# Kernel optimization log

Hardware: AMD Instinct MI355X
Metric: run time of the kernel (lower is better)

Reference implementation:

```python
import jax, jax.numpy as jnp
import numpy as np

N_NODES = 100000
N_EDGES = 1600000
IN_FEATS = 256
NUM_HEADS = 4
OUT_FEATS = 64
NEG_SLOPE = 0.2


def setup_inputs() -> dict:
    key = jax.random.key(0)
    k1, k2, k3, k4, k5, k6 = jax.random.split(key, 6)
    feat = jax.random.normal(k1, (N_NODES, IN_FEATS), dtype=jnp.float32)
    # VarianceScaling(scale=sqrt(2), fan_avg) ~ std = sqrt(2*sqrt(2)/(fan_in+fan_out))
    w_std = float(np.sqrt(np.sqrt(2.0) * 2.0 / (IN_FEATS + NUM_HEADS * OUT_FEATS)))
    W = jax.random.normal(k2, (IN_FEATS, NUM_HEADS * OUT_FEATS), dtype=jnp.float32) * w_std
    a_std = float(np.sqrt(np.sqrt(2.0) * 2.0 / (1 + OUT_FEATS)))
    attn_l = jax.random.normal(k3, (1, NUM_HEADS, OUT_FEATS), dtype=jnp.float32) * a_std
    attn_r = jax.random.normal(k4, (1, NUM_HEADS, OUT_FEATS), dtype=jnp.float32) * a_std
    src = jax.random.randint(k5, (N_EDGES,), 0, N_NODES, dtype=jnp.int32)
    dst = jax.random.randint(k6, (N_EDGES,), 0, N_NODES, dtype=jnp.int32)
    return {"feat": feat, "W": W, "attn_l": attn_l, "attn_r": attn_r, "src": src, "dst": dst}


def reference(feat, W, attn_l, attn_r, src, dst):
    N = feat.shape[0]
    H, D = attn_l.shape[1], attn_l.shape[2]
    # projection: [N, H, D]
    ft = jnp.reshape(feat @ W, (N, H, D))
    # per-node attention logits: [N, H]
    el = jnp.sum(ft * attn_l, axis=-1)
    er = jnp.sum(ft * attn_r, axis=-1)
    # per-edge logits (u_add_v) + LeakyReLU: [E, H]
    e = jax.nn.leaky_relu(el[src] + er[dst], negative_slope=NEG_SLOPE)
    # segmented softmax over incoming edges of each destination node
    seg_max = jax.ops.segment_max(e, dst, num_segments=N)  # [N, H]
    seg_max = jnp.where(jnp.isfinite(seg_max), seg_max, 0.0)
    ex = jnp.exp(e - seg_max[dst])  # [E, H]
    seg_sum = jax.ops.segment_sum(ex, dst, num_segments=N)  # [N, H]
    a = ex / seg_sum[dst]  # [E, H]
    # weighted scatter-sum aggregation (u_mul_e then sum): [N, H, D]
    msgs = ft[src] * a[:, :, None]  # [E, H, D]
    rst = jax.ops.segment_sum(msgs, dst, num_segments=N)
    return rst
```

## Files before the change

### kernel.cpp

```cpp
#include <hip/hip_runtime.h>

#define HEADS 4
#define DH 64
#define NHID 256
#define KIN 256
#define NEG_SLOPE 0.2f
#define CAP 128
#define EPB 2048

typedef __attribute__((ext_vector_type(8))) short short8;
typedef __attribute__((ext_vector_type(4))) float f32x4;

__device__ inline float bf2f(unsigned short u) {
  union { unsigned int i; float f; } v; v.i = ((unsigned int)u) << 16; return v.f;
}
__device__ inline unsigned short f2bf(float f) {
  union { float f; unsigned int i; } v; v.f = f;
  unsigned int r = v.i + 0x7FFF + ((v.i >> 16) & 1);
  return (unsigned short)(r >> 16);
}

__global__ void k_cvtW(const float* __restrict__ W, unsigned short* __restrict__ Wt,
                       int* __restrict__ deg, int M) {
  int n = blockIdx.x, k = threadIdx.x;
  Wt[n * 256 + k] = f2bf(W[k * 256 + n]);
  for (int i = blockIdx.x * 256 + threadIdx.x; i < M; i += 256 * 256) deg[i] = 0;
}

__global__ __launch_bounds__(256, 2) void k_fillgemm(
    const float* __restrict__ feat, const unsigned short* __restrict__ Wt,
    const float* __restrict__ al, const float* __restrict__ ar,
    unsigned short* __restrict__ ftb, float* __restrict__ el,
    float* __restrict__ er, int M,
    const int* __restrict__ src, const int* __restrict__ dst,
    int* __restrict__ deg, int* __restrict__ bucket, int E)
{
  __shared__ unsigned short As[64 * 256];
  __shared__ unsigned short Bs[2][256 * 32];
  const int t = threadIdx.x;
  const int b = blockIdx.x;
  const int q = b / 3, rmd = b % 3;

  if (rmd == 0) {
    int e0 = q * EPB + t;
    #pragma unroll
    for (int j = 0; j < 8; ++j) {
      int e = e0 + j * 256;
      if (e < E) {
        int d = __builtin_nontemporal_load(dst + e);
        int s = __builtin_nontemporal_load(src + e);
        int p = atomicAdd(&deg[d], 1);
        bucket[(size_t)d * CAP + p] = s;
      }
    }
    return;
  }

  const int gi = b - q - 1;
  const int lane = t & 63;
  const int w = t >> 6;
  const int row0 = gi * 64;

  f32x4 acc[4][4] = {};

  f32x4 av0[8], av1[8];
  #pragma unroll
  for (int j = 0; j < 8; ++j) {
    int g = j * 256 + t;
    int r = g >> 5, c = g & 31;
    const f32x4* ga = (const f32x4*)(feat + (size_t)min(row0 + r, M - 1) * KIN + c * 8);
    av0[j] = __builtin_nontemporal_load(ga);
    av1[j] = __builtin_nontemporal_load(ga + 1);
  }
  const int bn0 = t >> 2, bkc = t & 3;
  #pragma unroll
  for (int j = 0; j < 4; ++j) {
    int n = j * 64 + bn0;
    const unsigned short* gb = Wt + n * 256 + ((bkc ^ ((n >> 1) & 3)) * 8);
    __builtin_amdgcn_global_load_lds(
        (const __attribute__((address_space(1))) void*)gb,
        (__attribute__((address_space(3))) void*)((char*)Bs[0] + j * 4096 + t * 16),
        16, 0, 0);
  }
  #pragma unroll
  for (int j = 0; j < 8; ++j) {
    int g = j * 256 + t;
    int r = g >> 5, c = g & 31;
    short8 pk;
    pk[0] = (short)f2bf(av0[j][0]); pk[1] = (short)f2bf(av0[j][1]);
    pk[2] = (short)f2bf(av0[j][2]); pk[3] = (short)f2bf(av0[j][3]);
    pk[4] = (short)f2bf(av1[j][0]); pk[5] = (short)f2bf(av1[j][1]);
    pk[6] = (short)f2bf(av1[j][2]); pk[7] = (short)f2bf(av1[j][3]);
    *(short8*)((char*)As + r * 512 + ((c ^ (r & 7)) * 16)) = pk;
  }
  __syncthreads();

  const int i = lane & 15, kc = lane >> 4;
  for (int kt = 0; kt < 8; ++kt) {
    if (kt < 7) {
      int k0 = (kt + 1) * 32;
      #pragma unroll
      for (int j = 0; j < 4; ++j) {
        int n = j * 64 + bn0;
        const unsigned short* gb = Wt + n * 256 + k0 + ((bkc ^ ((n >> 1) & 3)) * 8);
        __builtin_amdgcn_global_load_lds(
            (const __attribute__((address_space(1))) void*)gb,
            (__attribute__((address_space(3))) void*)((char*)Bs[(kt + 1) & 1] + j * 4096 + t * 16),
            16, 0, 0);
      }
    }
    short8 af[4], bf[4];
    #pragma unroll
    for (int m = 0; m < 4; ++m) {
      int r = m * 16 + i;
      int c = kt * 4 + kc;
      af[m] = *(const short8*)((const char*)As + r * 512 + ((c ^ (r & 7)) * 16));
    }
    const char* bbase = (const char*)Bs[kt & 1];
    #pragma unroll
    for (int n = 0; n < 4; ++n) {
      int nr = w * 64 + n * 16 + i;
      bf[n] = *(const short8*)(bbase + nr * 64 + ((kc ^ ((nr >> 1) & 3)) * 16));
    }
    #pragma unroll
    for (int m = 0; m < 4; ++m)
      #pragma unroll
      for (int n = 0; n < 4; ++n)
        acc[m][n] = __builtin_amdgcn_mfma_f32_16x16x32_bf16(af[m], bf[n], acc[m][n], 0, 0, 0);
    __syncthreads();
  }

  const int ci = lane & 15, rg = lane >> 4;
  #pragma unroll
  for (int m = 0; m < 4; ++m) {
    #pragma unroll
    for (int r = 0; r < 4; ++r) {
      int grow = row0 + m * 16 + rg * 4 + r;
      if (grow < M) {
        unsigned short* fp = ftb + (size_t)grow * NHID + w * 64;
        #pragma unroll
        for (int n = 0; n < 4; ++n) fp[n * 16 + ci] = f2bf(acc[m][n][r]);
      }
    }
  }
  float alv[4], arv[4];
  #pragma unroll
  for (int n = 0; n < 4; ++n) {
    alv[n] = al[w * DH + n * 16 + ci];
    arv[n] = ar[w * DH + n * 16 + ci];
  }
  #pragma unroll
  for (int m = 0; m < 4; ++m) {
    #pragma unroll
    for (int r = 0; r < 4; ++r) {
      float pl = 0.f, pr = 0.f;
      #pragma unroll
      for (int n = 0; n < 4; ++n) {
        pl += acc[m][n][r] * alv[n];
        pr += acc[m][n][r] * arv[n];
      }
      pl += __shfl_xor(pl, 1); pl += __shfl_xor(pl, 2);
      pl += __shfl_xor(pl, 4); pl += __shfl_xor(pl, 8);
      pr += __shfl_xor(pr, 1); pr += __shfl_xor(pr, 2);
      pr += __shfl_xor(pr, 4); pr += __shfl_xor(pr, 8);
      if (ci == 0) {
        int grow = row0 + m * 16 + rg * 4 + r;
        if (grow < M) { el[grow * HEADS + w] = pl; er[grow * HEADS + w] = pr; }
      }
    }
  }
}

__global__ __launch_bounds__(256) void k_aggr(
    const unsigned short* __restrict__ ftb, const float* __restrict__ el,
    const float* __restrict__ er, const int* __restrict__ deg,
    const int* __restrict__ bucket, float* __restrict__ out, int N)
{
  int n = blockIdx.x * 4 + (threadIdx.x >> 6);
  int lane = threadIdx.x & 63;
  if (n >= N) return;
  int q  = lane >> 4;
  int ql = lane & 15;
  int hh = ql >> 2;
  int start = n * CAP;
  int end = start + deg[n];
  const short8* ft8 = (const short8*)ftb;
  float acc[16] = {};
  float ws = 0.f;
  if (end > start) {
    float erh = er[n * HEADS + hh];
    int last = end - 1;
    int eA = start + q;
    int eB = eA + 4;
    int sB = bucket[min(eB, last)];
    {
      int sA = bucket[min(eA, last)];
      float lxA = el[sA * 4 + hh];
      short8 fa0 = ft8[(size_t)sA * 32 + ql * 2];
      short8 fa1 = ft8[(size_t)sA * 32 + ql * 2 + 1];
      for (int e0 = start; e0 < end; e0 += 4) {
        int sC = bucket[min(e0 + 8 + q, last)];
        float lxB = el[sB * 4 + hh];
        short8 fb0 = ft8[(size_t)sB * 32 + ql * 2];
        short8 fb1 = ft8[(size_t)sB * 32 + ql * 2 + 1];
        bool v = (e0 + q) < end;
        float x = lxA + erh;
        x = x > 0.f ? x : NEG_SLOPE * x;
        float ex = v ? __expf(x) : 0.f;
        ws += ex;
        #pragma unroll
        for (int j = 0; j < 8; ++j) acc[j]     += ex * bf2f((unsigned short)fa0[j]);
        #pragma unroll
        for (int j = 0; j < 8; ++j) acc[j + 8] += ex * bf2f((unsigned short)fa1[j]);
        sB = sC; lxA = lxB; fa0 = fb0; fa1 = fb1;
      }
    }
  }
  ws += __shfl_xor(ws, 16); ws += __shfl_xor(ws, 32);
  #pragma unroll
  for (int j = 0; j < 16; ++j) {
    acc[j] += __shfl_xor(acc[j], 16);
    acc[j] += __shfl_xor(acc[j], 32);
  }
  if (q == 0) {
    float inv = (end > start) ? 1.f / ws : 0.f;
    float* op = out + (size_t)n * NHID + ql * 16;
    #pragma unroll
    for (int j4 = 0; j4 < 4; ++j4)
      *(float4*)(op + j4 * 4) = make_float4(acc[j4 * 4] * inv, acc[j4 * 4 + 1] * inv,
                                            acc[j4 * 4 + 2] * inv, acc[j4 * 4 + 3] * inv);
  }
}

extern "C" void kernel_launch(void* const* d_in, const int* in_sizes, int n_in,
                              void* d_out, int out_size, void* d_ws, size_t ws_size,
                              hipStream_t stream)
{
  const float* feat = (const float*)d_in[0];
  const float* W    = (const float*)d_in[1];
  const float* al   = (const float*)d_in[2];
  const float* ar   = (const float*)d_in[3];
  const int*   src  = (const int*)d_in[4];
  const int*   dst  = (const int*)d_in[5];
  const int M = in_sizes[0] / KIN;
  const int E = in_sizes[4];
  float* out = (float*)d_out;

  char* base = (char*)d_ws;
  size_t off = 0;
  auto alloc = [&](size_t b) { char* p = base + off; off = (off + b + 255) & ~(size_t)255; return p; };
  unsigned short* ftb = (unsigned short*)alloc((size_t)M * NHID * sizeof(unsigned short));
  unsigned short* Wt  = (unsigned short*)alloc(256 * 256 * sizeof(unsigned short));
  float* el     = (float*)alloc((size_t)M * HEADS * sizeof(float));
  float* er     = (float*)alloc((size_t)M * HEADS * sizeof(float));
  int*   deg    = (int*)alloc((size_t)M * sizeof(int));
  int*   bucket = (int*)alloc((size_t)M * CAP * sizeof(int));
  (void)ws_size; (void)n_in; (void)out_size;

  k_cvtW<<<256, 256, 0, stream>>>(W, Wt, deg, M);
  int nF = (E + EPB - 1) / EPB;
  int nG = (M + 63) / 64;
  k_fillgemm<<<nF + nG, 256, 0, stream>>>(feat, Wt, al, ar, ftb, el, er, M,
                                          src, dst, deg, bucket, E);
  k_aggr<<<(M + 3) / 4, 256, 0, stream>>>(ftb, el, er, deg, bucket, out, M);
}
```

Before: 253.6 us.

## Read W fragments directly from global memory and drop LDS staging for B

Removes the double-buffered shared-memory staging of the transposed weight matrix and has each wave load its B fragments straight from global (cache-resident) memory. This drops the per-k-step block barriers and halves the LDS footprint, which together with splitting the feature load into two halves (fewer live registers) allows raising launch bounds to three blocks per CU. The trade-off is more global/L2 traffic for W with load latency no longer hidden by prefetch.

```diff
diff --git a/kernel.cpp b/kernel.cpp
--- a/kernel.cpp
+++ b/kernel.cpp
@@ -27,7 +27,7 @@
   for (int i = blockIdx.x * 256 + threadIdx.x; i < M; i += 256 * 256) deg[i] = 0;
 }
 
-__global__ __launch_bounds__(256, 2) void k_fillgemm(
+__global__ __launch_bounds__(256, 3) void k_fillgemm(
     const float* __restrict__ feat, const unsigned short* __restrict__ Wt,
     const float* __restrict__ al, const float* __restrict__ ar,
     unsigned short* __restrict__ ftb, float* __restrict__ el,
@@ -36,7 +36,6 @@
     int* __restrict__ deg, int* __restrict__ bucket, int E)
 {
   __shared__ unsigned short As[64 * 256];
-  __shared__ unsigned short Bs[2][256 * 32];
   const int t = threadIdx.x;
   const int b = blockIdx.x;
   const int q = b / 3, rmd = b % 3;
@@ -63,71 +62,50 @@
 
   f32x4 acc[4][4] = {};
 
-  f32x4 av0[8], av1[8];
-  #pragma unroll
-  for (int j = 0; j < 8; ++j) {
-    int g = j * 256 + t;
-    int r = g >> 5, c = g & 31;
-    const f32x4* ga = (const f32x4*)(feat + (size_t)min(row0 + r, M - 1) * KIN + c * 8);
-    av0[j] = __builtin_nontemporal_load(ga);
-    av1[j] = __builtin_nontemporal_load(ga + 1);
-  }
-  const int bn0 = t >> 2, bkc = t & 3;
-  #pragma unroll
-  for (int j = 0; j < 4; ++j) {
-    int n = j * 64 + bn0;
-    const unsigned short* gb = Wt + n * 256 + ((bkc ^ ((n >> 1) & 3)) * 8);
-    __builtin_amdgcn_global_load_lds(
-        (const __attribute__((address_space(1))) void*)gb,
-        (__attribute__((address_space(3))) void*)((char*)Bs[0] + j * 4096 + t * 16),
-        16, 0, 0);
-  }
-  #pragma unroll
-  for (int j = 0; j < 8; ++j) {
-    int g = j * 256 + t;
-    int r = g >> 5, c = g & 31;
-    short8 pk;
-    pk[0] = (short)f2bf(av0[j][0]); pk[1] = (short)f2bf(av0[j][1]);
-    pk[2] = (short)f2bf(av0[j][2]); pk[3] = (short)f2bf(av0[j][3]);
-    pk[4] = (short)f2bf(av1[j][0]); pk[5] = (short)f2bf(av1[j][1]);
-    pk[6] = (short)f2bf(av1[j][2]); pk[7] = (short)f2bf(av1[j][3]);
-    *(short8*)((char*)As + r * 512 + ((c ^ (r & 7)) * 16)) = pk;
+  #pragma unroll
+  for (int p = 0; p < 2; ++p) {
+    f32x4 av0[4], av1[4];
+    #pragma unroll
+    for (int j = 0; j < 4; ++j) {
+      int g = (p * 4 + j) * 256 + t;
+      int r = g >> 5, c = g & 31;
+      const f32x4* ga = (const f32x4*)(feat + (size_t)min(row0 + r, M - 1) * KIN + c * 8);
+      av0[j] = __builtin_nontemporal_load(ga);
+      av1[j] = __builtin_nontemporal_load(ga + 1);
+    }
+    #pragma unroll
+    for (int j = 0; j < 4; ++j) {
+      int g = (p * 4 + j) * 256 + t;
+      int r = g >> 5, c = g & 31;
+      short8 pk;
+      pk[0] = (short)f2bf(av0[j][0]); pk[1] = (short)f2bf(av0[j][1]);
+      pk[2] = (short)f2bf(av0[j][2]); pk[3] = (short)f2bf(av0[j][3]);
+      pk[4] = (short)f2bf(av1[j][0]); pk[5] = (short)f2bf(av1[j][1]);
+      pk[6] = (short)f2bf(av1[j][2]); pk[7] = (short)f2bf(av1[j][3]);
+      *(short8*)((char*)As + r * 512 + ((c ^ (r & 7)) * 16)) = pk;
+    }
   }
   __syncthreads();
 
   const int i = lane & 15, kc = lane >> 4;
   for (int kt = 0; kt < 8; ++kt) {
-    if (kt < 7) {
-      int k0 = (kt + 1) * 32;
-      #pragma unroll
-      for (int j = 0; j < 4; ++j) {
-        int n = j * 64 + bn0;
-        const unsigned short* gb = Wt + n * 256 + k0 + ((bkc ^ ((n >> 1) & 3)) * 8);
-        __builtin_amdgcn_global_load_lds(
-            (const __attribute__((address_space(1))) void*)gb,
-            (__attribute__((address_space(3))) void*)((char*)Bs[(kt + 1) & 1] + j * 4096 + t * 16),
-            16, 0, 0);
-      }
-    }
     short8 af[4], bf[4];
+    #pragma unroll
+    for (int n = 0; n < 4; ++n) {
+      int nr = w * 64 + n * 16 + i;
+      bf[n] = *(const short8*)(Wt + nr * 256 + kt * 32 + kc * 8);
+    }
     #pragma unroll
     for (int m = 0; m < 4; ++m) {
       int r = m * 16 + i;
       int c = kt * 4 + kc;
       af[m] = *(const short8*)((const char*)As + r * 512 + ((c ^ (r & 7)) * 16));
     }
-    const char* bbase = (const char*)Bs[kt & 1];
-    #pragma unroll
-    for (int n = 0; n < 4; ++n) {
-      int nr = w * 64 + n * 16 + i;
-      bf[n] = *(const short8*)(bbase + nr * 64 + ((kc ^ ((nr >> 1) & 3)) * 16));
-    }
     #pragma unroll
     for (int m = 0; m < 4; ++m)
       #pragma unroll
       for (int n = 0; n < 4; ++n)
         acc[m][n] = __builtin_amdgcn_mfma_f32_16x16x32_bf16(af[m], bf[n], acc[m][n], 0, 0, 0);
-    __syncthreads();
   }
 
   const int ci = lane & 15, rg = lane >> 4;
```

Measured after the change: 272.0 us. +7.3%, slower.
